# Kernel tuning notes

Measured on AMD Instinct MI355X. Metric: run time of the kernel, lower is better.

The kernel has to match this reference:

```python
import jax, jax.numpy as jnp
import numpy as np

B, C, H, W = 16, 96, 96, 96
K, N, R, CR = 4, 8, 6, 12  # scan dirs, d_state, dt_rank, SE hidden


def channel_ln(x, g, b, eps=1e-6):
    # LayerNorm over channel dim (channel_first)
    mu = jnp.mean(x, axis=1, keepdims=True)
    var = jnp.var(x, axis=1, keepdims=True)
    return (x - mu) * jax.lax.rsqrt(var + eps) * g[None, :, None, None] + b[None, :, None, None]


def conv1x1(x, w, b):
    return jnp.einsum('bchw,dc->bdhw', x, w) + b[None, :, None, None]


def ss2d(x, xproj_w, dtproj_w, dtproj_b, A_logs, Ds, g, bta):
    # 4-direction selective scan (VMamba SS2D core). x: (B,C,H,W)
    Bq, Cq, Hq, Wq = x.shape
    L = Hq * Wq
    xf = x.reshape(Bq, Cq, L)
    xt = jnp.transpose(x, (0, 1, 3, 2)).reshape(Bq, Cq, L)
    xs = jnp.stack([xf, xt, xf[..., ::-1], xt[..., ::-1]], axis=1)  # (B,K,C,L)
    x_dbl = jnp.einsum('bkcl,kdc->bkdl', xs, xproj_w)  # (B,K,R+2N,L)
    dts, Bs, Cs = jnp.split(x_dbl, [R, R + N], axis=2)
    delta = jax.nn.softplus(jnp.einsum('bkrl,kcr->bkcl', dts, dtproj_w) + dtproj_b[None, :, :, None])
    A = -jnp.exp(A_logs)  # (K,C,N)
    u_t = jnp.moveaxis(xs, -1, 0)   # (L,B,K,C)
    d_t = jnp.moveaxis(delta, -1, 0)
    B_t = jnp.moveaxis(Bs, -1, 0)   # (L,B,K,N)
    C_t = jnp.moveaxis(Cs, -1, 0)
    h0 = jnp.zeros((Bq, K, Cq, N), x.dtype)

    @jax.checkpoint
    def step(h, inp):
        u, d, Bv, Cv = inp
        dA = jnp.exp(d[..., None] * A)                      # (B,K,C,N)
        h = dA * h + (d * u)[..., None] * Bv[:, :, None, :]
        return h, jnp.sum(h * Cv[:, :, None, :], axis=-1)   # (B,K,C)

    _, ys = jax.lax.scan(step, h0, (u_t, d_t, B_t, C_t))
    ys = jnp.moveaxis(ys, 0, -1) + Ds[None, :, :, None] * xs  # (B,K,C,L)

    def untrans(yk):
        return jnp.transpose(yk.reshape(Bq, Cq, Wq, Hq), (0, 1, 3, 2)).reshape(Bq, Cq, L)

    out = ys[:, 0] + untrans(ys[:, 1]) + ys[:, 2, :, ::-1] + untrans(ys[:, 3][..., ::-1])
    return channel_ln(out.reshape(Bq, Cq, Hq, Wq), g, bta)


def block_forward(x, ln_g, ln_b, p1_w, p1_b, p2in_w, p2in_b, dw_w, dw_b,
                  xproj_w, dtproj_w, dtproj_b, A_logs, Ds, ssln_g, ssln_b,
                  p2n_g, p2n_b, ca_w1, ca_b1, ca_w2, ca_b2, block_idx):
    h = channel_ln(x, ln_g, ln_b)
    a = jax.nn.silu(conv1x1(h, p1_w, p1_b))
    z = conv1x1(h, p2in_w, p2in_b)
    z = jax.lax.conv_general_dilated(z, dw_w, (1, 1), 'SAME',
                                     dimension_numbers=('NCHW', 'OIHW', 'NCHW'),
                                     feature_group_count=z.shape[1]) + dw_b[None, :, None, None]
    z = jax.nn.silu(z)
    if block_idx % 2 == 0:
        z = jnp.transpose(z, (0, 1, 3, 2))
    else:
        z = z[:, :, ::-1, ::-1]
    z = ss2d(z, xproj_w, dtproj_w, dtproj_b, A_logs, Ds, ssln_g, ssln_b)
    if block_idx % 2 == 0:
        z = jnp.transpose(z, (0, 1, 3, 2))
    else:
        z = z[:, :, ::-1, ::-1]
    z = channel_ln(z, p2n_g, p2n_b)
    y = a * z
    # channel attention (SE)
    s = jnp.mean(y, axis=(2, 3))  # (B,C)
    att = jax.nn.sigmoid(jnp.einsum('cr,br->bc', ca_w2,
                                    jax.nn.silu(jnp.einsum('rc,bc->br', ca_w1, s) + ca_b1)) + ca_b2)
    return x + y * att[:, :, None, None]


def local_mamba(x, params, block_idx):
    b, c, h, w = x.shape
    h2, w2 = h // 2, w // 2
    qs = jnp.stack([x[:, :, :h2, :w2], x[:, :, :h2, w2:],
                    x[:, :, h2:, :w2], x[:, :, h2:, w2:]])  # (4,B,C,h2,w2)
    fn = lambda q, *p: block_forward(q, *p, block_idx)
    outs = jax.vmap(fn)(qs, *params)
    top = jnp.concatenate([outs[0], outs[1]], axis=3)
    bot = jnp.concatenate([outs[2], outs[3]], axis=3)
    return jnp.concatenate([top, bot], axis=2)


def setup_inputs() -> dict:
    key = jax.random.key(0)
    ks = jax.random.split(key, 12)
    rn = lambda k, shape, s=1.0: jax.random.normal(k, shape, jnp.float32) * s
    return dict(
        x=rn(ks[0], (B, C, H, W)),
        ln_g=jnp.ones((4, C)), ln_b=jnp.zeros((4, C)),
        p1_w=rn(ks[1], (4, C, C), C ** -0.5), p1_b=jnp.zeros((4, C)),
        p2in_w=rn(ks[2], (4, C, C), C ** -0.5), p2in_b=jnp.zeros((4, C)),
        dw_w=rn(ks[3], (4, C, 1, 3, 3), 1.0 / 3.0), dw_b=jnp.zeros((4, C)),
        xproj_w=rn(ks[4], (4, K, R + 2 * N, C), C ** -0.5),
        dtproj_w=rn(ks[5], (4, K, C, R), R ** -0.5),
        dtproj_b=rn(ks[6], (4, K, C), 0.1),
        A_logs=jax.random.uniform(ks[7], (4, K, C, N), jnp.float32, 0.0, 1.0),
        Ds=jnp.ones((4, K, C)),
        ssln_g=jnp.ones((4, C)), ssln_b=jnp.zeros((4, C)),
        p2n_g=jnp.ones((4, C)), p2n_b=jnp.zeros((4, C)),
        ca_w1=rn(ks[8], (4, CR, C), C ** -0.5), ca_b1=jnp.zeros((4, CR)),
        ca_w2=rn(ks[9], (4, C, CR), CR ** -0.5), ca_b2=jnp.zeros((4, C)),
        block_idx=0,
    )


def reference(x, ln_g, ln_b, p1_w, p1_b, p2in_w, p2in_b, dw_w, dw_b,
              xproj_w, dtproj_w, dtproj_b, A_logs, Ds, ssln_g, ssln_b,
              p2n_g, p2n_b, ca_w1, ca_b1, ca_w2, ca_b2, block_idx):
    params = (ln_g, ln_b, p1_w, p1_b, p2in_w, p2in_b, dw_w, dw_b,
              xproj_w, dtproj_w, dtproj_b, A_logs, Ds, ssln_g, ssln_b,
              p2n_g, p2n_b, ca_w1, ca_b1, ca_w2, ca_b2)
    return local_mamba(x, params, block_idx)
```

## Files before the change

kernel.cpp:

```cpp
#include <hip/hip_runtime.h>
#include <hip/hip_bf16.h>

#define BQ 16
#define CN 96
#define HQ 48
#define LL 2304
#define NK 4
#define RR 6
#define NNS 8
#define DPJ 22
#define CRr 12
#define LOG2E 1.4426950408889634f

using bf16 = __hip_bfloat16;

__device__ __forceinline__ float b2f(bf16 v) { return __bfloat162float(v); }
__device__ __forceinline__ bf16  f2b(float v){ return __float2bfloat16(v); }
__device__ __forceinline__ float bflo(unsigned u){ return __uint_as_float(u << 16); }
__device__ __forceinline__ float bfhi(unsigned u){ return __uint_as_float(u & 0xffff0000u); }
__device__ __forceinline__ float sigf(float x){ return 1.f / (1.f + __expf(-x)); }
__device__ __forceinline__ float siluf(float x){ return x / (1.f + __expf(-x)); }
__device__ __forceinline__ unsigned packbf(float a, float b){
    unsigned lo = (unsigned)__builtin_bit_cast(unsigned short, f2b(a));
    unsigned hi = (unsigned)__builtin_bit_cast(unsigned short, f2b(b));
    return lo | (hi << 16);
}
__device__ __forceinline__ unsigned rot16(unsigned u){ return (u >> 16) | (u << 16); }
__device__ __forceinline__ void unpack8(uint4 v, float* f){
    f[0]=bflo(v.x); f[1]=bfhi(v.x); f[2]=bflo(v.y); f[3]=bfhi(v.y);
    f[4]=bflo(v.z); f[5]=bfhi(v.z); f[6]=bflo(v.w); f[7]=bfhi(v.w);
}
__device__ __forceinline__ void unpack4(uint2 v, float* f){
    f[0]=bflo(v.x); f[1]=bfhi(v.x); f[2]=bflo(v.y); f[3]=bfhi(v.y);
}
__device__ __forceinline__ float fexp2(float x){
#if __has_builtin(__builtin_amdgcn_exp2f)
    return __builtin_amdgcn_exp2f(x);
#else
    return __expf(x * 0.6931471805599453f);
#endif
}
__device__ __forceinline__ float qxor(float v, int ctrl_b1){
    int x;
    if (ctrl_b1) x = __builtin_amdgcn_mov_dpp(__float_as_int(v), 0xB1, 0xF, 0xF, true);
    else         x = __builtin_amdgcn_mov_dpp(__float_as_int(v), 0x4E, 0xF, 0xF, true);
    return __int_as_float(x);
}

__global__ __launch_bounds__(192) void k_lnconv(
    const float* __restrict__ x, const float* __restrict__ ln_g, const float* __restrict__ ln_b,
    const float* __restrict__ p1w, const float* __restrict__ p1b,
    const float* __restrict__ p2w, const float* __restrict__ p2b,
    bf16* __restrict__ a_out, bf16* __restrict__ z0_out)
{
    const int hh2 = blockIdx.x;
    const int b = blockIdx.y, q = blockIdx.z;
    const int h0 = (q >> 1) * HQ, w0 = (q & 1) * HQ;
    const int tid = threadIdx.x;
    const int qb = q * BQ + b;

    __shared__ alignas(16) bf16 hn[CN * 96];
    __shared__ alignas(16) bf16 wl[CN * 200];
    __shared__ float mu[96], rs[96];
    __shared__ float pmu[192], pv2[192];

    for (int t = tid; t < CN * CN; t += 192) {
        int d = t / CN, c = t % CN;
        wl[c * 200 + d]      = f2b(p1w[(q * CN + d) * CN + c]);
        wl[c * 200 + 96 + d] = f2b(p2w[(q * CN + d) * CN + c]);
    }
    for (int t = tid; t < CN * 24; t += 192) {
        int c = t / 24, v = t % 24;
        int row = v / 12, col = (v % 12) * 4;
        float4 xv = *reinterpret_cast<const float4*>(
            &x[((b * CN + c) * 96 + h0 + 2 * hh2 + row) * 96 + w0 + col]);
        uint2 pk; pk.x = packbf(xv.x, xv.y); pk.y = packbf(xv.z, xv.w);
        *reinterpret_cast<uint2*>(&hn[c * 96 + v * 4]) = pk;
    }
    __syncthreads();
    {
        int p = tid % 96, half = tid / 96;
        float s = 0.f, s2 = 0.f;
        for (int c = half * 48; c < half * 48 + 48; ++c) {
            float v = b2f(hn[c * 96 + p]); s += v; s2 += v * v;
        }
        pmu[half * 96 + p] = s; pv2[half * 96 + p] = s2;
    }
    __syncthreads();
    if (tid < 96) {
        float s = pmu[tid] + pmu[96 + tid];
        float s2 = pv2[tid] + pv2[96 + tid];
        float m = s * (1.f / 96.f);
        float var = s2 * (1.f / 96.f) - m * m;
        mu[tid] = m; rs[tid] = rsqrtf(var + 1e-6f);
    }
    __syncthreads();
    for (int t = tid; t < CN * 96; t += 192) {
        int c = t / 96, p = t % 96;
        float g = ln_g[q * CN + c], bb = ln_b[q * CN + c];
        hn[t] = f2b((b2f(hn[t]) - mu[p]) * rs[p] * g + bb);
    }
    __syncthreads();
    const int rg = tid >> 3, pg = tid & 7;
    const int row0 = rg * 8, pp0 = pg * 12;
    float acc[8][12];
    #pragma unroll
    for (int i = 0; i < 8; ++i)
        #pragma unroll
        for (int j = 0; j < 12; ++j) acc[i][j] = 0.f;

    for (int c = 0; c < CN; ++c) {
        uint4 wv = *reinterpret_cast<const uint4*>(&wl[c * 200 + row0]);
        float w[8];
        w[0] = bflo(wv.x); w[1] = bfhi(wv.x);
        w[2] = bflo(wv.y); w[3] = bfhi(wv.y);
        w[4] = bflo(wv.z); w[5] = bfhi(wv.z);
        w[6] = bflo(wv.w); w[7] = bfhi(wv.w);
        uint2 ha = *reinterpret_cast<const uint2*>(&hn[c * 96 + pp0]);
        uint2 hb = *reinterpret_cast<const uint2*>(&hn[c * 96 + pp0 + 4]);
        uint2 hc = *reinterpret_cast<const uint2*>(&hn[c * 96 + pp0 + 8]);
        float hv[12];
        hv[0] = bflo(ha.x); hv[1] = bfhi(ha.x); hv[2]  = bflo(ha.y); hv[3]  = bfhi(ha.y);
        hv[4] = bflo(hb.x); hv[5] = bfhi(hb.x); hv[6]  = bflo(hb.y); hv[7]  = bfhi(hb.y);
        hv[8] = bflo(hc.x); hv[9] = bfhi(hc.x); hv[10] = bflo(hc.y); hv[11] = bfhi(hc.y);
        #pragma unroll
        for (int i = 0; i < 8; ++i)
            #pragma unroll
            for (int j = 0; j < 12; ++j)
                acc[i][j] = fmaf(w[i], hv[j], acc[i][j]);
    }
    const int lbase = (2 * hh2 + pp0 / 48) * 48 + (pp0 % 48);
    #pragma unroll
    for (int i = 0; i < 8; ++i) {
        int row = row0 + i;
        bool isA = row < 96;
        int d = isA ? row : row - 96;
        float bias = isA ? p1b[q * CN + d] : p2b[q * CN + d];
        int oidx = (qb * CN + d) * LL + lbase;
        float v[12];
        #pragma unroll
        for (int j = 0; j < 12; ++j) v[j] = acc[i][j] + bias;
        if (isA) {
            #pragma unroll
            for (int j = 0; j < 12; ++j) v[j] = siluf(v[j]);
        }
        uint2 w0p, w1p, w2p;
        w0p.x = packbf(v[0], v[1]);  w0p.y = packbf(v[2], v[3]);
        w1p.x = packbf(v[4], v[5]);  w1p.y = packbf(v[6], v[7]);
        w2p.x = packbf(v[8], v[9]);  w2p.y = packbf(v[10], v[11]);
        bf16* dst = isA ? a_out : z0_out;
        *reinterpret_cast<uint2*>(&dst[oidx])     = w0p;
        *reinterpret_cast<uint2*>(&dst[oidx + 4]) = w1p;
        *reinterpret_cast<uint2*>(&dst[oidx + 8]) = w2p;
    }
}

__global__ __launch_bounds__(256) void k_dwconv(
    const bf16* __restrict__ z0, const float* __restrict__ dww, const float* __restrict__ dwb,
    const int* __restrict__ bidx, bf16* __restrict__ zt, bf16* __restrict__ ztT)
{
    const int c = blockIdx.x, b = blockIdx.y, q = blockIdx.z;
    const int tid = threadIdx.x;
    const int base = ((q * BQ + b) * CN + c) * LL;
    __shared__ float zin[50 * 50];
    __shared__ float zo[48 * 49];
    if (tid < 196) {
        int idx;
        if (tid < 50)       idx = tid;
        else if (tid < 100) idx = 49 * 50 + (tid - 50);
        else if (tid < 148) idx = (tid - 99) * 50;
        else                idx = (tid - 147) * 50 + 49;
        zin[idx] = 0.f;
    }
    for (int t = tid; t < 288; t += 256) {
        uint4 v = *reinterpret_cast<const uint4*>(&z0[base + t * 8]);
        float f[8]; unpack8(v, f);
        int e0 = t * 8, row = e0 / 48, col = e0 % 48;
        float* dst = &zin[(row + 1) * 50 + col + 1];
        #pragma unroll
        for (int i = 0; i < 8; ++i) dst[i] = f[i];
    }
    float wk[9];
    #pragma unroll
    for (int i = 0; i < 9; ++i) wk[i] = dww[(q * CN + c) * 9 + i];
    const float bias = dwb[q * CN + c];
    __syncthreads();
    for (int t = tid; t < LL; t += 256) {
        int hh = t / 48, ww = t % 48;
        const float* z0r = &zin[hh * 50 + ww];
        float s = bias;
        s = fmaf(wk[0], z0r[0],        s);
        s = fmaf(wk[1], z0r[1],        s);
        s = fmaf(wk[2], z0r[2],        s);
        s = fmaf(wk[3], z0r[50],       s);
        s = fmaf(wk[4], z0r[51],       s);
        s = fmaf(wk[5], z0r[52],       s);
        s = fmaf(wk[6], z0r[100],      s);
        s = fmaf(wk[7], z0r[101],      s);
        s = fmaf(wk[8], z0r[102],      s);
        zo[hh * 49 + ww] = siluf(s);
    }
    __syncthreads();
    const bool even = ((bidx[0] & 1) == 0);
    for (int t = tid; t < LL; t += 256) {
        int i = t / 48, j = t % 48;
        float vz, vzT;
        if (even) { vz = zo[j * 49 + i];               vzT = zo[i * 49 + j]; }
        else      { vz = zo[(47 - i) * 49 + (47 - j)]; vzT = zo[(47 - j) * 49 + (47 - i)]; }
        zt[base + t]  = f2b(vz);
        ztT[base + t] = f2b(vzT);
    }
}

__global__ __launch_bounds__(256) void k_xdbl(
    const bf16* __restrict__ zt, const bf16* __restrict__ ztT,
    const float* __restrict__ xprojw, bf16* __restrict__ xdbl)
{
    const int lt = blockIdx.x, k = blockIdx.y, qb = blockIdx.z;
    const int tid = threadIdx.x;
    const int l0 = lt * 192;
    const int q = qb >> 4;
    __shared__ alignas(16) bf16 ul[CN * 200];
    __shared__ alignas(16) bf16 wl[CN * 24];
    const bf16* __restrict__ src = (k & 1) ? ztT : zt;
    const bool rev = (k >= 2);
    for (int t = tid; t < CN * 24; t += 256) {
        int cc = t / 24, j0 = (t % 24) * 8;
        uint4 v;
        if (!rev) {
            v = *reinterpret_cast<const uint4*>(&src[(size_t)(qb * CN + cc) * LL + l0 + j0]);
        } else {
            v = *reinterpret_cast<const uint4*>(&src[(size_t)(qb * CN + cc) * LL + (LL - (l0 + j0) - 8)]);
            uint4 r; r.x = rot16(v.w); r.y = rot16(v.z); r.z = rot16(v.y); r.w = rot16(v.x);
            v = r;
        }
        *reinterpret_cast<uint4*>(&ul[cc * 200 + j0]) = v;
    }
    for (int t = tid; t < DPJ * CN; t += 256) {
        int d = t / CN, c = t % CN;
        wl[c * 24 + d] = f2b(xprojw[(q * NK + k) * DPJ * CN + t]);
    }
    __syncthreads();
    if (tid < 176) {
        const int dp = tid / 16, lg = tid % 16;
        const int d0 = dp * 2, llp = lg * 12;
        float acc0[12], acc1[12];
        #pragma unroll
        for (int j = 0; j < 12; ++j) { acc0[j] = 0.f; acc1[j] = 0.f; }
        for (int c = 0; c < CN; ++c) {
            unsigned wv = *reinterpret_cast<const unsigned*>(&wl[c * 24 + d0]);
            float w0 = bflo(wv), w1 = bfhi(wv);
            uint2 ua = *reinterpret_cast<const uint2*>(&ul[c * 200 + llp]);
            uint2 ub = *reinterpret_cast<const uint2*>(&ul[c * 200 + llp + 4]);
            uint2 uc = *reinterpret_cast<const uint2*>(&ul[c * 200 + llp + 8]);
            float uf[12];
            unpack4(ua, uf); unpack4(ub, uf + 4); unpack4(uc, uf + 8);
            #pragma unroll
            for (int j = 0; j < 12; ++j) {
                acc0[j] = fmaf(w0, uf[j], acc0[j]);
                acc1[j] = fmaf(w1, uf[j], acc1[j]);
            }
        }
        int ob = (qb * NK + k) * DPJ * LL + l0 + llp;
        uint2 o0a, o0b, o0c, o1a, o1b, o1c;
        o0a.x = packbf(acc0[0], acc0[1]);  o0a.y = packbf(acc0[2], acc0[3]);
        o0b.x = packbf(acc0[4], acc0[5]);  o0b.y = packbf(acc0[6], acc0[7]);
        o0c.x = packbf(acc0[8], acc0[9]);  o0c.y = packbf(acc0[10], acc0[11]);
        o1a.x = packbf(acc1[0], acc1[1]);  o1a.y = packbf(acc1[2], acc1[3]);
        o1b.x = packbf(acc1[4], acc1[5]);  o1b.y = packbf(acc1[6], acc1[7]);
        o1c.x = packbf(acc1[8], acc1[9]);  o1c.y = packbf(acc1[10], acc1[11]);
        *reinterpret_cast<uint2*>(&xdbl[ob + d0 * LL])           = o0a;
        *reinterpret_cast<uint2*>(&xdbl[ob + d0 * LL + 4])       = o0b;
        *reinterpret_cast<uint2*>(&xdbl[ob + d0 * LL + 8])       = o0c;
        *reinterpret_cast<uint2*>(&xdbl[ob + (d0 + 1) * LL])     = o1a;
        *reinterpret_cast<uint2*>(&xdbl[ob + (d0 + 1) * LL + 4]) = o1b;
        *reinterpret_cast<uint2*>(&xdbl[ob + (d0 + 1) * LL + 8]) = o1c;
    }
}


#define SCAN_BARRIER() asm volatile("s_waitcnt lgkmcnt(0)\n\ts_barrier" ::: "memory")

#define UWORD(NUA, IDX) (((IDX) & 3) == 0 ? NUA[(IDX) >> 2].x : \
                         ((IDX) & 3) == 1 ? NUA[(IDX) >> 2].y : \
                         ((IDX) & 3) == 2 ? NUA[(IDX) >> 2].z : NUA[(IDX) >> 2].w)

#define ROT3(v) (v) = ((v) == 2) ? 0 : ((v) + 1)

__global__ __launch_bounds__(384) void k_scan(
    const bf16* __restrict__ zt, const bf16* __restrict__ ztT,
    const bf16* __restrict__ xdbl,
    const float* __restrict__ dtw_g, const float* __restrict__ dtb_g,
    const float* __restrict__ Alog_g, const float* __restrict__ Ds_g,
    bf16* __restrict__ ys)
{
    const int bid = blockIdx.x;
    const int ch2 = bid & 1, k = (bid >> 1) & 3, qb = bid >> 3, q = qb >> 4;
    const int qk = q * NK + k;
    const int tid = threadIdx.x;
    const bool isScan = (tid < 192);
    const int lt = isScan ? tid : (tid - 192);
    const int ca = lt >> 2, p = lt & 3;
    const int c = ch2 * 48 + ca;

    __shared__ float dd3[3][48 * 52];
    __shared__ float xr3[3][6 * 52];
    __shared__ float bcv3[3][48 * 16];

    const bf16* __restrict__ src = (k & 1) ? ztT : zt;
    const bool rev = (k >= 2);
    const int ja = p * 12;

    float wdt[6] = {0.f, 0.f, 0.f, 0.f, 0.f, 0.f};
    float dtbc = 0.f;
    if (!isScan) {
        const float* wp = dtw_g + (size_t)qk * CN * RR + c * RR;
        float2 wa = *reinterpret_cast<const float2*>(wp);
        float2 wb = *reinterpret_cast<const float2*>(wp + 2);
        float2 wc = *reinterpret_cast<const float2*>(wp + 4);
        wdt[0] = wa.x; wdt[1] = wa.y; wdt[2] = wb.x; wdt[3] = wb.y; wdt[4] = wc.x; wdt[5] = wc.y;
        dtbc = dtb_g[qk * CN + c];
    }
    const bool xload = (!isScan) && (lt < 132);
    const int vr = lt / 6, jx = (lt % 6) * 8;
    const bf16* gx = xdbl + (size_t)(qb * NK + k) * (DPJ * LL) + (size_t)vr * LL + jx;
    int bccol = 0;
    if (vr >= 6) {
        int v = vr - 6;
        int n = v & 7;
        bccol = (n >> 1) * 4 + ((v >= 8) ? 2 : 0) + (n & 1);
    }

    float A0L = 0.f, A1L = 0.f, Dc = 0.f;
    if (isScan) {
        A0L = -__expf(Alog_g[((size_t)qk * CN + c) * NNS + 2 * p])     * LOG2E;
        A1L = -__expf(Alog_g[((size_t)qk * CN + c) * NNS + 2 * p + 1]) * LOG2E;
        Dc = Ds_g[qk * CN + c];
    }
    float h0 = 0.f, h1 = 0.f;
    const bf16* gu = src + (size_t)(qb * CN + c) * LL + (rev ? (LL - 48) : 0);
    const int ustep = rev ? -48 : 48;
    bf16* yp = ys + (size_t)(qb * NK + k) * (CN * LL) + (size_t)c * LL;

    #define COMMIT_BLOCK(PXV, XRB, BCB) do {                                          \
        if (xload) {                                                                  \
            float g[8]; unpack8(PXV, g);                                              \
            if (vr < 6) {                                                             \
                *reinterpret_cast<float4*>(&(XRB)[vr * 52 + jx])                      \
                    = make_float4(g[0], g[1], g[2], g[3]);                            \
                *reinterpret_cast<float4*>(&(XRB)[vr * 52 + jx + 4])                  \
                    = make_float4(g[4], g[5], g[6], g[7]);                            \
            } else {                                                                  \
                _Pragma("unroll")                                                     \
                for (int i = 0; i < 8; ++i) (BCB)[(jx + i) * 16 + bccol] = g[i];      \
            }                                                                         \
        }                                                                             \
    } while (0)

    #define DELTA_BLOCK(XRB, DDB) do {                                                \
        float acc[12];                                                                \
        _Pragma("unroll")                                                             \
        for (int i = 0; i < 12; ++i) acc[i] = dtbc;                                   \
        _Pragma("unroll")                                                             \
        for (int r = 0; r < 6; ++r) {                                                 \
            float4 d0 = *reinterpret_cast<const float4*>(&(XRB)[r * 52 + ja]);        \
            float4 d1 = *reinterpret_cast<const float4*>(&(XRB)[r * 52 + ja + 4]);    \
            float4 d2 = *reinterpret_cast<const float4*>(&(XRB)[r * 52 + ja + 8]);    \
            float wr_ = wdt[r];                                                       \
            acc[0] = fmaf(wr_, d0.x, acc[0]);  acc[1] = fmaf(wr_, d0.y, acc[1]);      \
            acc[2] = fmaf(wr_, d0.z, acc[2]);  acc[3] = fmaf(wr_, d0.w, acc[3]);      \
            acc[4] = fmaf(wr_, d1.x, acc[4]);  acc[5] = fmaf(wr_, d1.y, acc[5]);      \
            acc[6] = fmaf(wr_, d1.z, acc[6]);  acc[7] = fmaf(wr_, d1.w, acc[7]);      \
            acc[8] = fmaf(wr_, d2.x, acc[8]);  acc[9] = fmaf(wr_, d2.y, acc[9]);      \
            acc[10] = fmaf(wr_, d2.z, acc[10]); acc[11] = fmaf(wr_, d2.w, acc[11]);   \
        }                                                                             \
        _Pragma("unroll")                                                             \
        for (int i = 0; i < 12; ++i) {                                                \
            float a = acc[i];                                                         \
            acc[i] = (a > 15.f) ? a : __logf(1.f + __expf(a));                        \
        }                                                                             \
        float4* dp = reinterpret_cast<float4*>(&(DDB)[ca * 52 + ja]);                 \
        dp[0] = make_float4(acc[0], acc[1], acc[2], acc[3]);                          \
        dp[1] = make_float4(acc[4], acc[5], acc[6], acc[7]);                          \
        dp[2] = make_float4(acc[8], acc[9], acc[10], acc[11]);                        \
    } while (0)

    uint4 u_a[6], u_b[6];
    uint4 px_a = {0,0,0,0}, px_b = {0,0,0,0}, px1 = {0,0,0,0};
    if (isScan) {
        #pragma unroll
        for (int i = 0; i < 6; ++i) u_a[i] = *reinterpret_cast<const uint4*>(gu + i * 8);
        gu += ustep;
        #pragma unroll
        for (int i = 0; i < 6; ++i) u_b[i] = *reinterpret_cast<const uint4*>(gu + i * 8);
        gu += ustep;
    } else {
        uint4 px0 = {0,0,0,0};
        if (xload) {
            px0  = *reinterpret_cast<const uint4*>(gx);
            px1  = *reinterpret_cast<const uint4*>(gx + 48);
            px_a = *reinterpret_cast<const uint4*>(gx + 96);
            px_b = *reinterpret_cast<const uint4*>(gx + 144);
            gx += 192;
        }
        COMMIT_BLOCK(px0, xr3[0], bcv3[0]);
    }
    SCAN_BARRIER();
    if (!isScan) {
        DELTA_BLOCK(xr3[0], dd3[0]);
        COMMIT_BLOCK(px1, xr3[1], bcv3[1]);
    }
    SCAN_BARRIER();

    int s_cur = 0;
    int d_idx = 1, c_idx = 2;

    #define PROD_BODY(CH, PX) do {                                                    \
        const int chp_ = (CH);                                                        \
        if (chp_ + 2 < 48) COMMIT_BLOCK(PX, xr3[c_idx], bcv3[c_idx]);                 \
        if (chp_ + 4 < 48 && xload) { PX = *reinterpret_cast<const uint4*>(gx); gx += 48; } \
        if (chp_ + 1 < 48) DELTA_BLOCK(xr3[d_idx], dd3[d_idx]);                       \
        ROT3(d_idx); ROT3(c_idx);                                                     \
    } while (0)

    #define SCAN_CHUNK(CH, UC) do {                                                   \
        const int ch_ = (CH);                                                         \
        uint4 nu[6];                                                                  \
        if (!rev) {                                                                   \
            nu[0] = UC[0]; nu[1] = UC[1]; nu[2] = UC[2];                              \
            nu[3] = UC[3]; nu[4] = UC[4]; nu[5] = UC[5];                              \
        } else {                                                                      \
            _Pragma("unroll")                                                         \
            for (int qq = 0; qq < 6; ++qq) {                                          \
                nu[qq].x = rot16(UC[5 - qq].w); nu[qq].y = rot16(UC[5 - qq].z);       \
                nu[qq].z = rot16(UC[5 - qq].y); nu[qq].w = rot16(UC[5 - qq].x);       \
            }                                                                         \
        }                                                                             \
        {                                                                             \
            const int l0 = ch_ * 48;                                                  \
            const float* ddc = &dd3[s_cur][ca * 52];                                  \
            const float* bcc = &bcv3[s_cur][p * 4];                                   \
            _Pragma("unroll")                                                         \
            for (int gg = 0; gg < 6; ++gg) {                                          \
                unsigned pk[4];                                                       \
                _Pragma("unroll")                                                     \
                for (int half = 0; half < 2; ++half) {                                \
                    const int j0 = gg * 8 + half * 4;                                 \
                    float4 d4 = *reinterpret_cast<const float4*>(ddc + j0);           \
                    const float* df = reinterpret_cast<const float*>(&d4);            \
                    _Pragma("unroll")                                                 \
                    for (int s = 0; s < 4; ++s) {                                     \
                        const int j = j0 + s;                                         \
                        const unsigned uwv = UWORD(nu, j >> 1);                       \
                        float u = (j & 1) ? bfhi(uwv) : bflo(uwv);                    \
                        float d = df[s];                                              \
                        float4 bq = *reinterpret_cast<const float4*>(bcc + j * 16);   \
                        float du = d * u;                                             \
                        float dA0 = fexp2(d * A0L);                                   \
                        float dA1 = fexp2(d * A1L);                                   \
                        h0 = fmaf(dA0, h0, du * bq.x);                                \
                        h1 = fmaf(dA1, h1, du * bq.y);                                \
                        float y = fmaf(h0, bq.z, h1 * bq.w);                          \
                        y += qxor(y, 1); y += qxor(y, 0);                             \
                        y = fmaf(Dc, u, y);                                           \
                        unsigned hb = (unsigned)__builtin_bit_cast(unsigned short, f2b(y)); \
                        const int sl = half * 4 + s;                                  \
                        if (sl & 1) pk[sl >> 1] |= hb << 16; else pk[sl >> 1] = hb;   \
                    }                                                                 \
                }                                                                     \
                if (p == 0) {                                                         \
                    uint4 wv4; wv4.x = pk[0]; wv4.y = pk[1]; wv4.z = pk[2]; wv4.w = pk[3]; \
                    *reinterpret_cast<uint4*>(yp + l0 + gg * 8) = wv4;                \
                }                                                                     \
            }                                                                         \
        }                                                                             \
        if (ch_ + 2 < 48) {                                                           \
            _Pragma("unroll")                                                         \
            for (int i = 0; i < 6; ++i) UC[i] = *reinterpret_cast<const uint4*>(gu + i * 8); \
            gu += ustep;                                                              \
        }                                                                             \
        ROT3(s_cur);                                                                  \
    } while (0)

    for (int t = 0; t < 24; ++t) {
        if (isScan) SCAN_CHUNK(2 * t, u_a);
        else        PROD_BODY(2 * t, px_a);
        SCAN_BARRIER();
        if (isScan) SCAN_CHUNK(2 * t + 1, u_b);
        else        PROD_BODY(2 * t + 1, px_b);
        SCAN_BARRIER();
    }

    #undef SCAN_CHUNK
    #undef PROD_BODY
    #undef DELTA_BLOCK
    #undef COMMIT_BLOCK
}

__global__ __launch_bounds__(256) void k_sum(
    const bf16* __restrict__ ys, bf16* __restrict__ s_out)
{
    const int c = blockIdx.x, b = blockIdx.y, q = blockIdx.z;
    const int qb = q * BQ + b;
    const int tid = threadIdx.x;
    __shared__ float t0[48 * 49];
    __shared__ float t2[48 * 49];
    const size_t base0 = ((size_t)(qb * NK + 0) * CN + c) * LL;
    const size_t base1 = ((size_t)(qb * NK + 1) * CN + c) * LL;
    const size_t base2 = ((size_t)(qb * NK + 2) * CN + c) * LL;
    const size_t base3 = ((size_t)(qb * NK + 3) * CN + c) * LL;
    for (int idx = tid; idx < 288; idx += 256) {
        int e0 = idx * 8, h = e0 / 48, w = e0 % 48;
        float f[8];
        unpack8(*reinterpret_cast<const uint4*>(&ys[base0 + e0]), f);
        #pragma unroll
        for (int i = 0; i < 8; ++i) t0[h * 49 + w + i] = f[i];
        unpack8(*reinterpret_cast<const uint4*>(&ys[base2 + e0]), f);
        #pragma unroll
        for (int i = 0; i < 8; ++i) t2[h * 49 + w + i] = f[i];
    }
    __syncthreads();
    const size_t cbase = ((size_t)qb * CN + c) * LL;
    for (int idx = tid; idx < 288; idx += 256) {
        int m0 = idx * 8, ww = m0 / 48, hh = m0 % 48;
        float f1[8], f3[8];
        unpack8(*reinterpret_cast<const uint4*>(&ys[base1 + m0]), f1);
        unpack8(*reinterpret_cast<const uint4*>(&ys[base3 + (LL - 8 - m0)]), f3);
        float o[8];
        #pragma unroll
        for (int i = 0; i < 8; ++i) {
            float v0 = t0[(hh + i) * 49 + ww];
            float v2 = t2[(47 - hh - i) * 49 + (47 - ww)];
            o[i] = v0 + f1[i] + v2 + f3[7 - i];
        }
        uint4 w;
        w.x = packbf(o[0], o[1]); w.y = packbf(o[2], o[3]);
        w.z = packbf(o[4], o[5]); w.w = packbf(o[6], o[7]);
        *reinterpret_cast<uint4*>(&s_out[cbase + m0]) = w;
    }
}

__global__ __launch_bounds__(256) void k_combine(
    const bf16* __restrict__ s_in, const bf16* __restrict__ a_in,
    const float* __restrict__ ssg, const float* __restrict__ ssb,
    const float* __restrict__ png, const float* __restrict__ pnb,
    const int* __restrict__ bidx,
    bf16* __restrict__ y_out, float* __restrict__ s_buf)
{
    const int ww = blockIdx.x, b = blockIdx.y, q = blockIdx.z;
    const int qb = q * BQ + b;
    const int tid = threadIdx.x;
    __shared__ float o[CN * 48];
    __shared__ float mu[48], rs[48];
    __shared__ float pp[192], pp2[192];
    for (int v = tid; v < 576; v += 256) {
        int e0 = v * 8, cc = e0 / 48, hh = e0 % 48;
        float f[8];
        unpack8(*reinterpret_cast<const uint4*>(&s_in[((size_t)qb * CN + cc) * LL + ww * 48 + hh]), f);
        #pragma unroll
        for (int i = 0; i < 8; ++i) o[cc * 48 + hh + i] = f[i];
    }
    __syncthreads();
    if (tid < 192) {
        int hh = tid % 48, part = tid / 48;
        float s = 0.f, s2 = 0.f;
        int c0 = part * 24;
        for (int cc = c0; cc < c0 + 24; ++cc) { float v = o[cc * 48 + hh]; s += v; s2 += v * v; }
        pp[tid] = s; pp2[tid] = s2;
    }
    __syncthreads();
    if (tid < 48) {
        float s = pp[tid] + pp[tid + 48] + pp[tid + 96] + pp[tid + 144];
        float s2 = pp2[tid] + pp2[tid + 48] + pp2[tid + 96] + pp2[tid + 144];
        float m = s * (1.f / 96.f), var = s2 * (1.f / 96.f) - m * m;
        mu[tid] = m; rs[tid] = rsqrtf(var + 1e-6f);
    }
    __syncthreads();
    for (int t = tid; t < CN * 48; t += 256) {
        int cc = t / 48, hh = t % 48;
        o[t] = (o[t] - mu[hh]) * rs[hh] * ssg[q * CN + cc] + ssb[q * CN + cc];
    }
    __syncthreads();
    if (tid < 192) {
        int hh = tid % 48, part = tid / 48;
        float s = 0.f, s2 = 0.f;
        int c0 = part * 24;
        for (int cc = c0; cc < c0 + 24; ++cc) { float v = o[cc * 48 + hh]; s += v; s2 += v * v; }
        pp[tid] = s; pp2[tid] = s2;
    }
    __syncthreads();
    if (tid < 48) {
        float s = pp[tid] + pp[tid + 48] + pp[tid + 96] + pp[tid + 144];
        float s2 = pp2[tid] + pp2[tid + 48] + pp2[tid + 96] + pp2[tid + 144];
        float m = s * (1.f / 96.f), var = s2 * (1.f / 96.f) - m * m;
        mu[tid] = m; rs[tid] = rsqrtf(var + 1e-6f);
    }
    __syncthreads();
    const bool even = ((bidx[0] & 1) == 0);
    if (even) {
        for (int v = tid; v < 576; v += 256) {
            int e0 = v * 8, cc = e0 / 48, hh = e0 % 48;
            size_t oidx = ((size_t)qb * CN + cc) * LL + ww * 48 + hh;
            float af[8];
            unpack8(*reinterpret_cast<const uint4*>(&a_in[oidx]), af);
            float yv[8];
            #pragma unroll
            for (int i = 0; i < 8; ++i) {
                float z2 = (o[cc * 48 + hh + i] - mu[hh + i]) * rs[hh + i] * png[q * CN + cc] + pnb[q * CN + cc];
                yv[i] = af[i] * z2;
                o[cc * 48 + hh + i] = yv[i];
            }
            uint4 w;
            w.x = packbf(yv[0], yv[1]); w.y = packbf(yv[2], yv[3]);
            w.z = packbf(yv[4], yv[5]); w.w = packbf(yv[6], yv[7]);
            *reinterpret_cast<uint4*>(&y_out[oidx]) = w;
        }
    } else {
        for (int t = tid; t < CN * 48; t += 256) {
            int cc = t / 48, hh = t % 48;
            float z2 = (o[t] - mu[hh]) * rs[hh] * png[q * CN + cc] + pnb[q * CN + cc];
            size_t oidx = ((size_t)qb * CN + cc) * LL + (47 - hh) * 48 + (47 - ww);
            float yv = b2f(a_in[oidx]) * z2;
            y_out[oidx] = f2b(yv);
            o[t] = yv;
        }
    }
    __syncthreads();
    if (tid < CN) {
        float s = 0.f;
        for (int j = 0; j < 48; ++j) s += o[tid * 48 + j];
        atomicAdd(&s_buf[qb * CN + tid], s);
    }
}

__global__ __launch_bounds__(256) void k_final(
    const float* __restrict__ x, const bf16* __restrict__ y_in,
    const float* __restrict__ s_buf,
    const float* __restrict__ w1, const float* __restrict__ b1,
    const float* __restrict__ w2, const float* __restrict__ b2,
    float* __restrict__ out)
{
    const int c = blockIdx.x, b = blockIdx.y, q = blockIdx.z;
    const int h0 = (q >> 1) * HQ, w0 = (q & 1) * HQ;
    const int qb = q * BQ + b;
    const int tid = threadIdx.x;
    __shared__ float tl[CRr];
    __shared__ float tpart[16 * CRr];
    __shared__ float attv;
    if (tid < 192) {
        int r = tid % CRr, part = tid / CRr;
        float acc = 0.f;
        const float* wr = w1 + (q * CRr + r) * CN;
        const float* sb = s_buf + qb * CN;
        int c0 = part * 6;
        for (int cc = c0; cc < c0 + 6; ++cc)
            acc = fmaf(wr[cc], sb[cc] * (1.f / (float)LL), acc);
        tpart[part * CRr + r] = acc;
    }
    __syncthreads();
    if (tid < CRr) {
        float acc = b1[q * CRr + tid];
        #pragma unroll
        for (int pt = 0; pt < 16; ++pt) acc += tpart[pt * CRr + tid];
        tl[tid] = siluf(acc);
    }
    __syncthreads();
    if (tid == 0) {
        float acc = b2[q * CN + c];
        #pragma unroll
        for (int r = 0; r < CRr; ++r) acc = fmaf(w2[(q * CN + c) * CRr + r], tl[r], acc);
        attv = sigf(acc);
    }
    __syncthreads();
    const float av = attv;
    const size_t ybase = (size_t)(qb * CN + c) * LL;
    const int xb = (b * CN + c) * 9216 + h0 * 96 + w0;
    for (int t = tid; t < LL / 8; t += 256) {
        int e0 = t * 8;
        int gi = xb + (e0 / 48) * 96 + (e0 % 48);
        uint4 yv = *reinterpret_cast<const uint4*>(&y_in[ybase + e0]);
        float yf[8]; unpack8(yv, yf);
        float4 xa = *reinterpret_cast<const float4*>(&x[gi]);
        float4 xc = *reinterpret_cast<const float4*>(&x[gi + 4]);
        float4 o0 = {xa.x + yf[0]*av, xa.y + yf[1]*av, xa.z + yf[2]*av, xa.w + yf[3]*av};
        float4 o1 = {xc.x + yf[4]*av, xc.y + yf[5]*av, xc.z + yf[6]*av, xc.w + yf[7]*av};
        *reinterpret_cast<float4*>(&out[gi])     = o0;
        *reinterpret_cast<float4*>(&out[gi + 4]) = o1;
    }
}

extern "C" void kernel_launch(void* const* d_in, const int* in_sizes, int n_in,
                              void* d_out, int out_size, void* d_ws, size_t ws_size,
                              hipStream_t stream)
{
    (void)in_sizes; (void)n_in; (void)out_size; (void)ws_size;
    const float* x       = (const float*)d_in[0];
    const float* ln_g    = (const float*)d_in[1];
    const float* ln_b    = (const float*)d_in[2];
    const float* p1_w    = (const float*)d_in[3];
    const float* p1_b    = (const float*)d_in[4];
    const float* p2in_w  = (const float*)d_in[5];
    const float* p2in_b  = (const float*)d_in[6];
    const float* dw_w    = (const float*)d_in[7];
    const float* dw_b    = (const float*)d_in[8];
    const float* xproj_w = (const float*)d_in[9];
    const float* dtproj_w= (const float*)d_in[10];
    const float* dtproj_b= (const float*)d_in[11];
    const float* A_logs  = (const float*)d_in[12];
    const float* Ds      = (const float*)d_in[13];
    const float* ssln_g  = (const float*)d_in[14];
    const float* ssln_b  = (const float*)d_in[15];
    const float* p2n_g   = (const float*)d_in[16];
    const float* p2n_b   = (const float*)d_in[17];
    const float* ca_w1   = (const float*)d_in[18];
    const float* ca_b1   = (const float*)d_in[19];
    const float* ca_w2   = (const float*)d_in[20];
    const float* ca_b2   = (const float*)d_in[21];
    const int*  bidx     = (const int*)d_in[22];
    float* out = (float*)d_out;

    char* ws = (char*)d_ws;
    const size_t off_a    = 0;
    const size_t off_zt   = 28311552;
    const size_t off_ztT  = 56623104;
    const size_t off_xdbl = 84934656;
    const size_t off_ys   = 110886912;
    const size_t off_z0   = off_ys;
    const size_t off_s    = off_zt;
    const size_t off_y    = off_ztT;
    const size_t off_sb   = 224133120;

    bf16*  a_buf   = (bf16*)(ws + off_a);
    bf16*  zt_buf  = (bf16*)(ws + off_zt);
    bf16*  ztT_buf = (bf16*)(ws + off_ztT);
    bf16*  xdbl_buf= (bf16*)(ws + off_xdbl);
    bf16*  ys_buf  = (bf16*)(ws + off_ys);
    bf16*  z0_buf  = (bf16*)(ws + off_z0);
    bf16*  s_sum   = (bf16*)(ws + off_s);
    bf16*  y_buf   = (bf16*)(ws + off_y);
    float* s_buf   = (float*)(ws + off_sb);

    (void)hipMemsetAsync(ws + off_sb, 0, 24576, stream);

    k_lnconv<<<dim3(24, 16, 4), 192, 0, stream>>>(
        x, ln_g, ln_b, p1_w, p1_b, p2in_w, p2in_b, a_buf, z0_buf);
    k_dwconv<<<dim3(96, 16, 4), 256, 0, stream>>>(
        z0_buf, dw_w, dw_b, bidx, zt_buf, ztT_buf);
    k_xdbl<<<dim3(12, 4, 64), 256, 0, stream>>>(
        zt_buf, ztT_buf, xproj_w, xdbl_buf);
    k_scan<<<dim3(512), 384, 0, stream>>>(
        zt_buf, ztT_buf, xdbl_buf, dtproj_w, dtproj_b, A_logs, Ds, ys_buf);
    k_sum<<<dim3(96, 16, 4), 256, 0, stream>>>(
        ys_buf, s_sum);
    k_combine<<<dim3(48, 16, 4), 256, 0, stream>>>(
        s_sum, a_buf, ssln_g, ssln_b, p2n_g, p2n_b, bidx, y_buf, s_buf);
    k_final<<<dim3(96, 16, 4), 256, 0, stream>>>(
        x, y_buf, s_buf, ca_w1, ca_b1, ca_w2, ca_b2, out);
}
```

Baseline: 729.3 us.

## Use MFMA bf16 matrix cores for fused LN + dual 1x1 conv in k_lnconv

Rewrites the k_lnconv GEMM, which computes the two 1x1 convs as a 192x96x96 product, to use 16x16x32 bf16 MFMA instructions instead of scalar FMAs. Weights and activations move to row-major LDS tiles with a 104-element padded stride, and channel statistics are read with vectorized loads. Bias and LN parameters are cached in LDS. The cost is scalar transposed LDS stores when loading x, and 2-byte scattered global stores in the epilogue instead of packed vector stores.

New measurement: 632.8 us. 13.2% less time.

```diff
diff --git a/kernel.cpp b/kernel.cpp
--- a/kernel.cpp
+++ b/kernel.cpp
@@ -13,6 +13,9 @@
 #define LOG2E 1.4426950408889634f
 
 using bf16 = __hip_bfloat16;
+
+typedef __attribute__((ext_vector_type(8))) short bf16x8;
+typedef __attribute__((ext_vector_type(4))) float f32x4;
 
 __device__ __forceinline__ float b2f(bf16 v) { return __bfloat162float(v); }
 __device__ __forceinline__ bf16  f2b(float v){ return __float2bfloat16(v); }
@@ -59,30 +62,45 @@
     const int tid = threadIdx.x;
     const int qb = q * BQ + b;
 
-    __shared__ alignas(16) bf16 hn[CN * 96];
-    __shared__ alignas(16) bf16 wl[CN * 200];
+    __shared__ alignas(16) bf16 wl2[192 * 104];
+    __shared__ alignas(16) bf16 hn2[96 * 104];
     __shared__ float mu[96], rs[96];
     __shared__ float pmu[192], pv2[192];
-
-    for (int t = tid; t < CN * CN; t += 192) {
-        int d = t / CN, c = t % CN;
-        wl[c * 200 + d]      = f2b(p1w[(q * CN + d) * CN + c]);
-        wl[c * 200 + 96 + d] = f2b(p2w[(q * CN + d) * CN + c]);
-    }
+    __shared__ float biasLds[192];
+    __shared__ float gl[96], bl[96];
+
+    for (int t = tid; t < 192 * 24; t += 192) {
+        int row = t / 24, c4 = (t % 24) * 4;
+        const float* srcw = (row < 96) ? &p1w[(q * CN + row) * CN + c4]
+                                       : &p2w[(q * CN + (row - 96)) * CN + c4];
+        float4 wv = *reinterpret_cast<const float4*>(srcw);
+        uint2 pk; pk.x = packbf(wv.x, wv.y); pk.y = packbf(wv.z, wv.w);
+        *reinterpret_cast<uint2*>(&wl2[row * 104 + c4]) = pk;
+    }
+    if (tid < 192)
+        biasLds[tid] = (tid < 96) ? p1b[q * CN + tid] : p2b[q * CN + (tid - 96)];
+    if (tid < 96) { gl[tid] = ln_g[q * CN + tid]; bl[tid] = ln_b[q * CN + tid]; }
     for (int t = tid; t < CN * 24; t += 192) {
         int c = t / 24, v = t % 24;
         int row = v / 12, col = (v % 12) * 4;
+        int p = row * 48 + col;
         float4 xv = *reinterpret_cast<const float4*>(
             &x[((b * CN + c) * 96 + h0 + 2 * hh2 + row) * 96 + w0 + col]);
-        uint2 pk; pk.x = packbf(xv.x, xv.y); pk.y = packbf(xv.z, xv.w);
-        *reinterpret_cast<uint2*>(&hn[c * 96 + v * 4]) = pk;
+        hn2[p * 104 + c]       = f2b(xv.x);
+        hn2[(p + 1) * 104 + c] = f2b(xv.y);
+        hn2[(p + 2) * 104 + c] = f2b(xv.z);
+        hn2[(p + 3) * 104 + c] = f2b(xv.w);
     }
     __syncthreads();
     {
         int p = tid % 96, half = tid / 96;
+        const bf16* hp = &hn2[p * 104 + half * 48];
         float s = 0.f, s2 = 0.f;
-        for (int c = half * 48; c < half * 48 + 48; ++c) {
-            float v = b2f(hn[c * 96 + p]); s += v; s2 += v * v;
+        #pragma unroll
+        for (int c8 = 0; c8 < 48; c8 += 8) {
+            float f[8]; unpack8(*reinterpret_cast<const uint4*>(hp + c8), f);
+            #pragma unroll
+            for (int i = 0; i < 8; ++i) { s += f[i]; s2 += f[i] * f[i]; }
         }
         pmu[half * 96 + p] = s; pv2[half * 96 + p] = s2;
     }
@@ -95,63 +113,68 @@
         mu[tid] = m; rs[tid] = rsqrtf(var + 1e-6f);
     }
     __syncthreads();
-    for (int t = tid; t < CN * 96; t += 192) {
-        int c = t / 96, p = t % 96;
-        float g = ln_g[q * CN + c], bb = ln_b[q * CN + c];
-        hn[t] = f2b((b2f(hn[t]) - mu[p]) * rs[p] * g + bb);
-    }
-    __syncthreads();
-    const int rg = tid >> 3, pg = tid & 7;
-    const int row0 = rg * 8, pp0 = pg * 12;
-    float acc[8][12];
+    for (int t = tid; t < 96 * 12; t += 192) {
+        int p = t / 12, c8 = (t % 12) * 8;
+        float f[8]; unpack8(*reinterpret_cast<const uint4*>(&hn2[p * 104 + c8]), f);
+        float m = mu[p], r = rs[p];
+        unsigned ou[4];
+        #pragma unroll
+        for (int i = 0; i < 8; i += 2) {
+            float v0 = (f[i]     - m) * r * gl[c8 + i]     + bl[c8 + i];
+            float v1 = (f[i + 1] - m) * r * gl[c8 + i + 1] + bl[c8 + i + 1];
+            ou[i >> 1] = packbf(v0, v1);
+        }
+        uint4 ov; ov.x = ou[0]; ov.y = ou[1]; ov.z = ou[2]; ov.w = ou[3];
+        *reinterpret_cast<uint4*>(&hn2[p * 104 + c8]) = ov;
+    }
+    __syncthreads();
+    const int w = tid >> 6;
+    const int l = tid & 63;
+    const int lr = l & 15;
+    const int lq = l >> 4;
+    f32x4 acc[4][6];
     #pragma unroll
-    for (int i = 0; i < 8; ++i)
-        #pragma unroll
-        for (int j = 0; j < 12; ++j) acc[i][j] = 0.f;
-
-    for (int c = 0; c < CN; ++c) {
-        uint4 wv = *reinterpret_cast<const uint4*>(&wl[c * 200 + row0]);
-        float w[8];
-        w[0] = bflo(wv.x); w[1] = bfhi(wv.x);
-        w[2] = bflo(wv.y); w[3] = bfhi(wv.y);
-        w[4] = bflo(wv.z); w[5] = bfhi(wv.z);
-        w[6] = bflo(wv.w); w[7] = bfhi(wv.w);
-        uint2 ha = *reinterpret_cast<const uint2*>(&hn[c * 96 + pp0]);
-        uint2 hb = *reinterpret_cast<const uint2*>(&hn[c * 96 + pp0 + 4]);
-        uint2 hc = *reinterpret_cast<const uint2*>(&hn[c * 96 + pp0 + 8]);
-        float hv[12];
-        hv[0] = bflo(ha.x); hv[1] = bfhi(ha.x); hv[2]  = bflo(ha.y); hv[3]  = bfhi(ha.y);
-        hv[4] = bflo(hb.x); hv[5] = bfhi(hb.x); hv[6]  = bflo(hb.y); hv[7]  = bfhi(hb.y);
-        hv[8] = bflo(hc.x); hv[9] = bfhi(hc.x); hv[10] = bflo(hc.y); hv[11] = bfhi(hc.y);
-        #pragma unroll
-        for (int i = 0; i < 8; ++i)
+    for (int m = 0; m < 4; ++m)
+        #pragma unroll
+        for (int n = 0; n < 6; ++n)
+            acc[m][n] = (f32x4){0.f, 0.f, 0.f, 0.f};
+    #pragma unroll
+    for (int k0 = 0; k0 < 96; k0 += 32) {
+        bf16x8 afr[4], bfr[6];
+        #pragma unroll
+        for (int m = 0; m < 4; ++m)
+            afr[m] = *reinterpret_cast<const bf16x8*>(
+                &wl2[(w * 64 + m * 16 + lr) * 104 + k0 + lq * 8]);
+        #pragma unroll
+        for (int n = 0; n < 6; ++n)
+            bfr[n] = *reinterpret_cast<const bf16x8*>(
+                &hn2[(n * 16 + lr) * 104 + k0 + lq * 8]);
+        #pragma unroll
+        for (int m = 0; m < 4; ++m)
             #pragma unroll
-            for (int j = 0; j < 12; ++j)
-                acc[i][j] = fmaf(w[i], hv[j], acc[i][j]);
-    }
-    const int lbase = (2 * hh2 + pp0 / 48) * 48 + (pp0 % 48);
+            for (int n = 0; n < 6; ++n)
+                acc[m][n] = __builtin_amdgcn_mfma_f32_16x16x32_bf16(
+                    afr[m], bfr[n], acc[m][n], 0, 0, 0);
+    }
     #pragma unroll
-    for (int i = 0; i < 8; ++i) {
-        int row = row0 + i;
-        bool isA = row < 96;
-        int d = isA ? row : row - 96;
-        float bias = isA ? p1b[q * CN + d] : p2b[q * CN + d];
-        int oidx = (qb * CN + d) * LL + lbase;
-        float v[12];
-        #pragma unroll
-        for (int j = 0; j < 12; ++j) v[j] = acc[i][j] + bias;
-        if (isA) {
+    for (int m = 0; m < 4; ++m) {
+        const int Rbase = w * 64 + m * 16 + lq * 4;
+        #pragma unroll
+        for (int n = 0; n < 6; ++n) {
+            const int col = n * 16 + lr;
+            const int colin = (col >= 48) ? (col - 48) : col;
+            const int lbase = (2 * hh2 + (col >= 48 ? 1 : 0)) * 48 + colin;
             #pragma unroll
-            for (int j = 0; j < 12; ++j) v[j] = siluf(v[j]);
-        }
-        uint2 w0p, w1p, w2p;
-        w0p.x = packbf(v[0], v[1]);  w0p.y = packbf(v[2], v[3]);
-        w1p.x = packbf(v[4], v[5]);  w1p.y = packbf(v[6], v[7]);
-        w2p.x = packbf(v[8], v[9]);  w2p.y = packbf(v[10], v[11]);
-        bf16* dst = isA ? a_out : z0_out;
-        *reinterpret_cast<uint2*>(&dst[oidx])     = w0p;
-        *reinterpret_cast<uint2*>(&dst[oidx + 4]) = w1p;
-        *reinterpret_cast<uint2*>(&dst[oidx + 8]) = w2p;
+            for (int r = 0; r < 4; ++r) {
+                const int R = Rbase + r;
+                const bool isA = R < 96;
+                const int d = isA ? R : R - 96;
+                float v = acc[m][n][r] + biasLds[R];
+                if (isA) v = siluf(v);
+                bf16* dst = isA ? a_out : z0_out;
+                dst[(size_t)(qb * CN + d) * LL + lbase] = f2b(v);
+            }
+        }
     }
 }
 
```
